# Kernel tuning notes

Hardware: AMD Instinct MI355X
Metric: run time of the kernel (lower is better)

The kernel has to match this reference:

```python
import jax, jax.numpy as jnp
import numpy as np

B, N, K = 2, 10000, 20
C_EDGE = [(4, 64), (64, 64), (64, 128), (128, 128)]  # (Cin, Cout) per edge conv
C_CAT = 64 + 64 + 128 + 128  # 384
C5 = 512
C_FEAT = [128, 128, 256]
NUM_CLASSES = 20


def _neighbor_idx(n, k):
    # idx[i] = torch.roll(arange(n), shifts=i)[:k]  ->  idx[i, j] = (j - i) mod n
    return (jnp.arange(k)[None, :] - jnp.arange(n)[:, None]) % n  # (N, K)


def _edge_conv(x, w, s, t, idx):
    # x: (B, C, N); w: (Co, 2C); s, t: (Co,) folded eval-mode BN scale/shift
    xn = x[:, :, idx]                                  # neighbor gather (B, C, N, K)
    ctr = jnp.broadcast_to(x[:, :, :, None], xn.shape)  # center repeat (B, C, N, K)
    e = jnp.concatenate([ctr - xn, ctr], axis=1)        # edge feature (B, 2C, N, K)
    y = jnp.einsum('oc,bcnk->bonk', w, e)               # 1x1 conv
    y = y * s[None, :, None, None] + t[None, :, None, None]
    y = jnp.where(y > 0, y, 0.2 * y)                    # LeakyReLU(0.2)
    return jnp.max(y, axis=-1)                          # max over K -> (B, Co, N)


def _conv1d_bn(x, w, s, t):
    # x: (B, C, N); 1x1 conv1d + folded BN
    return jnp.einsum('oc,bcn->bon', w, x) * s[None, :, None] + t[None, :, None]


def setup_inputs() -> dict:
    key = jax.random.key(0)
    ks = iter(jax.random.split(key, 64))
    d = {
        'coords': jax.random.normal(next(ks), (B, N, 3), jnp.float32),
        'feats': jax.random.normal(next(ks), (B, N, 4), jnp.float32),
    }
    def conv_bn(cin, cout):
        w = jax.random.normal(next(ks), (cout, cin), jnp.float32) / np.sqrt(cin).astype(np.float32)
        s = 0.75 + 0.5 * jax.random.uniform(next(ks), (cout,), jnp.float32)
        t = 0.1 * jax.random.normal(next(ks), (cout,), jnp.float32)
        return w, s, t
    for i, (ci, co) in enumerate(C_EDGE, 1):
        d[f'ew{i}'], d[f'es{i}'], d[f'et{i}'] = conv_bn(2 * ci, co)
    d['w5'], d['s5'], d['t5'] = conv_bn(C_CAT, C5)
    for i, cf in enumerate(C_FEAT, 1):
        d[f'fw{i}'], d[f'fs{i}'], d[f'ft{i}'] = conv_bn(C5, cf)
    d['sem_w'] = jax.random.normal(next(ks), (NUM_CLASSES, C_FEAT[-1]), jnp.float32) / np.sqrt(C_FEAT[-1]).astype(np.float32)
    d['sem_b'] = jnp.zeros((NUM_CLASSES,), jnp.float32)
    return d


def reference(coords, feats,
              ew1, es1, et1, ew2, es2, et2, ew3, es3, et3, ew4, es4, et4,
              w5, s5, t5,
              fw1, fs1, ft1, fw2, fs2, ft2, fw3, fs3, ft3,
              sem_w, sem_b):
    # x = cat(coords, intensity) -> (B, 4, N)
    x = jnp.concatenate([coords, feats[:, :, 3:4]], axis=-1).transpose(0, 2, 1)
    idx = _neighbor_idx(N, K)
    x1 = _edge_conv(x, ew1, es1, et1, idx)
    x2 = _edge_conv(x1, ew2, es2, et2, idx)
    x3 = _edge_conv(x2, ew3, es3, et3, idx)
    x4 = _edge_conv(x3, ew4, es4, et4, idx)
    xc = jnp.concatenate([x1, x2, x3, x4], axis=1)       # (B, 384, N)
    y = _conv1d_bn(xc, w5, s5, t5)
    y = jnp.where(y > 0, y, 0.2 * y)                      # conv5 activation
    f1 = _conv1d_bn(y, fw1, fs1, ft1).transpose(0, 2, 1)  # (B, N, 128)
    f2 = _conv1d_bn(y, fw2, fs2, ft2).transpose(0, 2, 1)  # (B, N, 128)
    f3 = _conv1d_bn(y, fw3, fs3, ft3).transpose(0, 2, 1)  # (B, N, 256)
    sem_logits = f3 @ sem_w.T + sem_b                     # (B, N, 20)
    masks = jnp.zeros((B, N), dtype=bool)                 # no padding: N == num_points
    return (f1, f2, f3, coords, masks, sem_logits)
```

## Files before the change

kernel.cpp:

```cpp
#include <hip/hip_runtime.h>

#define N_PTS 10000
#define NBATCH 2
#define COLS (N_PTS * NBATCH)
#define COLSP 20096

typedef __attribute__((ext_vector_type(8))) short bf16x8;
typedef __attribute__((ext_vector_type(4))) float f32x4;

static __device__ __forceinline__ float leaky(float v) { return v > 0.f ? v : 0.2f * v; }

static __device__ __forceinline__ unsigned short f2b(float x) {
  unsigned int u = __float_as_uint(x);
  unsigned int r = (u + 0x7fffu + ((u >> 16) & 1u)) >> 16;
  return (unsigned short)r;
}
static __device__ __forceinline__ float b2f(unsigned short h) {
  return __uint_as_float((unsigned int)h << 16);
}

static __device__ __forceinline__ void prep_one(const float* __restrict__ ew,
                                                float* __restrict__ WS, int O, int C, int i) {
  int o = i / C, c = i - o * C;
  float wa = ew[(size_t)o * 2 * C + c];
  float wb = ew[(size_t)o * 2 * C + C + c];
  WS[(size_t)o * C + c] = wa + wb;
  WS[(size_t)(O + o) * C + c] = wa;
}

__global__ void prep_all(const float* __restrict__ coords, const float* __restrict__ feats,
                         float* __restrict__ X0, const float* __restrict__ ew1,
                         float* __restrict__ WS1, const float* __restrict__ ew2,
                         float* __restrict__ WS2, const float* __restrict__ ew3,
                         float* __restrict__ WS3, const float* __restrict__ ew4,
                         float* __restrict__ WS4) {
  int i = blockIdx.x * 256 + threadIdx.x;
  if (i < COLS) {
    const float* cp = coords + (size_t)i * 3;
    X0[0 * COLS + i] = cp[0];
    X0[1 * COLS + i] = cp[1];
    X0[2 * COLS + i] = cp[2];
    X0[3 * COLS + i] = feats[(size_t)i * 4 + 3];
    return;
  }
  i -= COLS;
  if (i < 256) { prep_one(ew1, WS1, 64, 4, i); return; }
  i -= 256;
  if (i < 4096) { prep_one(ew2, WS2, 64, 64, i); return; }
  i -= 4096;
  if (i < 8192) { prep_one(ew3, WS3, 128, 64, i); return; }
  i -= 8192;
  if (i < 16384) { prep_one(ew4, WS4, 128, 128, i); return; }
}

template <int K, int MODE>
__global__ __launch_bounds__(256) void gemm_kernel(
    const float* __restrict__ W, const float* __restrict__ X, float* __restrict__ Out,
    const float* __restrict__ s, const float* __restrict__ t, int Cf) {
  __shared__ float Ws[32][68];
  __shared__ float Xs[32][132];
  const int tid = threadIdx.x;
  const int col0 = blockIdx.x * 128;
  const int row0 = blockIdx.y * 64;
  const int tn = tid & 31, tm = tid >> 5;
  float acc[8][4];
#pragma unroll
  for (int i = 0; i < 8; i++)
#pragma unroll
    for (int j = 0; j < 4; j++) acc[i][j] = 0.f;

  const bool colok = (col0 + tn * 4) < COLS;

  for (int k0 = 0; k0 < K; k0 += 32) {
    {
      int m = tid >> 2;
      int kq = (tid & 3) * 8;
      if ((K & 31) == 0) {
        const float* wp = W + (size_t)(row0 + m) * K + k0 + kq;
        float4 w0 = *(const float4*)wp;
        float4 w1 = *(const float4*)(wp + 4);
        Ws[kq + 0][m] = w0.x; Ws[kq + 1][m] = w0.y; Ws[kq + 2][m] = w0.z; Ws[kq + 3][m] = w0.w;
        Ws[kq + 4][m] = w1.x; Ws[kq + 5][m] = w1.y; Ws[kq + 6][m] = w1.z; Ws[kq + 7][m] = w1.w;
      } else {
#pragma unroll
        for (int j = 0; j < 8; j++) {
          int k = kq + j;
          Ws[k][m] = (k0 + k < K) ? W[(size_t)(row0 + m) * K + k0 + k] : 0.f;
        }
      }
    }
#pragma unroll
    for (int p = 0; p < 4; p++) {
      int idx = tid + p * 256;
      int k = idx >> 5;
      int n4 = (idx & 31) << 2;
      int col = col0 + n4;
      float4 v = make_float4(0.f, 0.f, 0.f, 0.f);
      if (k0 + k < K && col < COLS) v = *(const float4*)(X + (size_t)(k0 + k) * COLS + col);
      *(float4*)&Xs[k][n4] = v;
    }
    __syncthreads();
#pragma unroll
    for (int k = 0; k < 32; k++) {
      float a[8], b[4];
      *(float4*)&a[0] = *(const float4*)&Ws[k][tm * 8];
      *(float4*)&a[4] = *(const float4*)&Ws[k][tm * 8 + 4];
      *(float4*)&b[0] = *(const float4*)&Xs[k][tn * 4];
#pragma unroll
      for (int i = 0; i < 8; i++)
#pragma unroll
        for (int j = 0; j < 4; j++) acc[i][j] = fmaf(a[i], b[j], acc[i][j]);
    }
    __syncthreads();
  }

  if (colok) {
#pragma unroll
    for (int i = 0; i < 8; i++) {
      int row = row0 + tm * 8 + i;
      float4 v = make_float4(acc[i][0], acc[i][1], acc[i][2], acc[i][3]);
      *(float4*)(Out + (size_t)row * COLS + col0 + tn * 4) = v;
    }
  }
}

__global__ __launch_bounds__(256) void edge_finish(const float* __restrict__ AB, int O,
                                                   const float* __restrict__ s,
                                                   const float* __restrict__ t,
                                                   float* __restrict__ Xout) {
  __shared__ float sh[1024 + 20];
  int o = blockIdx.y;
  int b = blockIdx.z;
  int n0 = blockIdx.x * 1024;
  int nb = min(1024, N_PTS - n0);
  const float* Bt = AB + (size_t)(O + o) * COLS + (size_t)b * N_PTS;
  int base = N_PTS - n0 - nb + 1;
  int L = nb + 19;
  for (int i = threadIdx.x; i < L; i += 256) {
    int p = base + i;
    if (p >= N_PTS) p -= N_PTS;
    sh[i] = Bt[p];
  }
  __syncthreads();
  const float* Arow = AB + (size_t)o * COLS + (size_t)b * N_PTS;
  float ss = s[o], tt = t[o];
  for (int d = threadIdx.x; d < nb; d += 256) {
    int w = nb - 1 - d;
    float mn = sh[w];
#pragma unroll
    for (int k = 1; k < 20; k++) mn = fminf(mn, sh[w + k]);
    float v = (Arow[n0 + d] - mn) * ss + tt;
    Xout[(size_t)o * COLS + (size_t)b * N_PTS + n0 + d] = leaky(v);
  }
}

__global__ void sem_prep(const float* __restrict__ sem_w, const float* __restrict__ sem_b,
                         const float* __restrict__ fw3, const float* __restrict__ fs3,
                         const float* __restrict__ ft3, float* __restrict__ SWp,
                         float* __restrict__ biasp) {
  int i = blockIdx.x * blockDim.x + threadIdx.x;
  if (i < 20 * 512) {
    int cls = i / 512, k = i - cls * 512;
    float acc = 0.f;
    for (int c = 0; c < 256; c++) acc += sem_w[cls * 256 + c] * fs3[c] * fw3[(size_t)c * 512 + k];
    SWp[i] = acc;
  }
  if (i < 20) {
    float acc = sem_b[i];
    for (int c = 0; c < 256; c++) acc += sem_w[i * 256 + c] * ft3[c];
    biasp[i] = acc;
  }
}

__global__ void split_w5(const float* __restrict__ w5, unsigned short* __restrict__ Wc) {
  int i = blockIdx.x * 256 + threadIdx.x;
  if (i >= 512 * 384) return;
  int m = i / 384, k = i - m * 384;
  float w = w5[i];
  unsigned short hi = f2b(w);
  unsigned short lo = f2b(w - b2f(hi));
  unsigned short* row = Wc + (size_t)m * 1152;
  row[k] = hi;
  row[384 + k] = hi;
  row[768 + k] = lo;
}

__global__ void split_wf(const float* __restrict__ fw1, const float* __restrict__ fw2,
                         const float* __restrict__ fw3, const float* __restrict__ SWp,
                         const float* __restrict__ fs1, const float* __restrict__ ft1,
                         const float* __restrict__ fs2, const float* __restrict__ ft2,
                         const float* __restrict__ fs3, const float* __restrict__ ft3,
                         const float* __restrict__ Bp, unsigned short* __restrict__ Wc,
                         float* __restrict__ sF, float* __restrict__ tF) {
  int i = blockIdx.x * 256 + threadIdx.x;
  if (i >= 640 * 512) return;
  int m = i >> 9, k = i & 511;
  float w = 0.f, sv = 0.f, tv = 0.f;
  if (m < 128) {
    w = fw1[(size_t)m * 512 + k]; sv = fs1[m]; tv = ft1[m];
  } else if (m < 256) {
    w = fw2[(size_t)(m - 128) * 512 + k]; sv = fs2[m - 128]; tv = ft2[m - 128];
  } else if (m < 512) {
    w = fw3[(size_t)(m - 256) * 512 + k]; sv = fs3[m - 256]; tv = ft3[m - 256];
  } else if (m < 532) {
    w = SWp[(size_t)(m - 512) * 512 + k]; sv = 1.f; tv = Bp[m - 512];
  }
  unsigned short hi = f2b(w);
  unsigned short lo = f2b(w - b2f(hi));
  unsigned short* row = Wc + (size_t)m * 1536;
  row[k] = hi;
  row[512 + k] = hi;
  row[1024 + k] = lo;
  if (k == 0) { sF[m] = sv; tF[m] = tv; }
}

__global__ __launch_bounds__(256) void xpose_split(const float* __restrict__ XC,
                                                   unsigned short* __restrict__ XCt) {
  __shared__ float tile[32][65];
  int n0 = blockIdx.x * 64;
  int c0 = blockIdx.y * 32;
#pragma unroll
  for (int i = 0; i < 8; i++) {
    int e = threadIdx.x + i * 256;
    int c = e >> 6, n = e & 63;
    float v = 0.f;
    if (n0 + n < COLS) v = XC[(size_t)(c0 + c) * COLS + n0 + n];
    tile[c][n] = v;
  }
  __syncthreads();
#pragma unroll
  for (int i = 0; i < 2; i++) {
    int e = threadIdx.x + i * 256;
    int n = e >> 3, cq = (e & 7) * 4;
    if (n0 + n >= COLS) continue;
    unsigned short h[4], l[4];
#pragma unroll
    for (int j = 0; j < 4; j++) {
      float v = tile[cq + j][n];
      h[j] = f2b(v);
      l[j] = f2b(v - b2f(h[j]));
    }
    unsigned short* op = XCt + (size_t)(n0 + n) * 768 + c0 + cq;
    *(ushort4*)op = make_ushort4(h[0], h[1], h[2], h[3]);
    *(ushort4*)(op + 384) = make_ushort4(l[0], l[1], l[2], l[3]);
  }
}

template <int KP, int KX, int XSTR, int MODE>
__global__ __launch_bounds__(256) void mgemm(
    const unsigned short* __restrict__ Wc, const unsigned short* __restrict__ Xt,
    float* __restrict__ O0, float* __restrict__ O1, float* __restrict__ O2,
    float* __restrict__ O3, unsigned short* __restrict__ Yt, const float* __restrict__ s,
    const float* __restrict__ t) {
  __shared__ unsigned short Al[128 * 32];
  __shared__ unsigned short Bl[128 * 32];
  const int tid = threadIdx.x;
  const int wid = tid >> 6, lane = tid & 63;
  const int col0 = blockIdx.x * 128;
  const int row0 = blockIdx.y * 128;
  const int wm = wid >> 1, wn = wid & 1;
  f32x4 acc[4][4];
  f32x4 z = {0.f, 0.f, 0.f, 0.f};
#pragma unroll
  for (int i = 0; i < 4; i++)
#pragma unroll
    for (int j = 0; j < 4; j++) acc[i][j] = z;

  for (int k0 = 0; k0 < KP; k0 += 32) {
    int xoff = (k0 < 2 * KX) ? k0 : k0 - 2 * KX;
#pragma unroll
    for (int p = 0; p < 2; p++) {
      int idx = tid + p * 256;
      int r = idx >> 2, jj = idx & 3;
      int js = jj ^ ((r >> 1) & 3);
      __builtin_amdgcn_global_load_lds(
          (const __attribute__((address_space(1))) unsigned int*)(Wc + (size_t)(row0 + r) * KP +
                                                                  k0 + js * 8),
          (__attribute__((address_space(3))) unsigned int*)(Al + idx * 8), 16, 0, 0);
      __builtin_amdgcn_global_load_lds(
          (const __attribute__((address_space(1))) unsigned int*)(Xt + (size_t)(col0 + r) * XSTR +
                                                                  xoff + js * 8),
          (__attribute__((address_space(3))) unsigned int*)(Bl + idx * 8), 16, 0, 0);
    }
    __syncthreads();
    bf16x8 a[4], b[4];
#pragma unroll
    for (int f = 0; f < 4; f++) {
      int m = wm * 64 + f * 16 + (lane & 15);
      int ja = (lane >> 4) ^ ((m >> 1) & 3);
      a[f] = *(const bf16x8*)(Al + m * 32 + ja * 8);
      int n = wn * 64 + f * 16 + (lane & 15);
      int jb = (lane >> 4) ^ ((n >> 1) & 3);
      b[f] = *(const bf16x8*)(Bl + n * 32 + jb * 8);
    }
#pragma unroll
    for (int i = 0; i < 4; i++)
#pragma unroll
      for (int j = 0; j < 4; j++)
        acc[i][j] = __builtin_amdgcn_mfma_f32_16x16x32_bf16(a[i], b[j], acc[i][j], 0, 0, 0);
    __syncthreads();
  }

#pragma unroll
  for (int j = 0; j < 4; j++) {
    int n = col0 + wn * 64 + j * 16 + (lane & 15);
    if (n >= COLS) continue;
#pragma unroll
    for (int i = 0; i < 4; i++) {
      int mb = row0 + wm * 64 + i * 16 + 4 * (lane >> 4);
      if (MODE == 0) {
        unsigned short h[4], l[4];
#pragma unroll
        for (int r = 0; r < 4; r++) {
          float v = acc[i][j][r] * s[mb + r] + t[mb + r];
          v = leaky(v);
          h[r] = f2b(v);
          l[r] = f2b(v - b2f(h[r]));
        }
        unsigned short* yp = Yt + (size_t)n * 1024 + mb;
        *(ushort4*)yp = make_ushort4(h[0], h[1], h[2], h[3]);
        *(ushort4*)(yp + 512) = make_ushort4(l[0], l[1], l[2], l[3]);
      } else {
        float4 v;
        v.x = acc[i][j][0] * s[mb + 0] + t[mb + 0];
        v.y = acc[i][j][1] * s[mb + 1] + t[mb + 1];
        v.z = acc[i][j][2] * s[mb + 2] + t[mb + 2];
        v.w = acc[i][j][3] * s[mb + 3] + t[mb + 3];
        float* p;
        if (mb < 128)
          p = O0 + (size_t)n * 128 + mb;
        else if (mb < 256)
          p = O1 + (size_t)n * 128 + (mb - 128);
        else if (mb < 512)
          p = O2 + (size_t)n * 256 + (mb - 256);
        else if (mb < 532)
          p = O3 + (size_t)n * 20 + (mb - 512);
        else
          continue;
        *(float4*)p = v;
      }
    }
  }
}

__global__ void misc_kernel(const float* __restrict__ coords, float* __restrict__ out_coords,
                            float* __restrict__ out_masks) {
  int i = blockIdx.x * blockDim.x + threadIdx.x;
  if (i < NBATCH * N_PTS * 3) out_coords[i] = coords[i];
  if (i < NBATCH * N_PTS) out_masks[i] = 0.f;
}

extern "C" void kernel_launch(void* const* d_in, const int* in_sizes, int n_in, void* d_out,
                              int out_size, void* d_ws, size_t ws_size, hipStream_t stream) {
  const float* coords = (const float*)d_in[0];
  const float* feats = (const float*)d_in[1];
  const float* ew1 = (const float*)d_in[2];
  const float* es1 = (const float*)d_in[3];
  const float* et1 = (const float*)d_in[4];
  const float* ew2 = (const float*)d_in[5];
  const float* es2 = (const float*)d_in[6];
  const float* et2 = (const float*)d_in[7];
  const float* ew3 = (const float*)d_in[8];
  const float* es3 = (const float*)d_in[9];
  const float* et3 = (const float*)d_in[10];
  const float* ew4 = (const float*)d_in[11];
  const float* es4 = (const float*)d_in[12];
  const float* et4 = (const float*)d_in[13];
  const float* w5 = (const float*)d_in[14];
  const float* s5 = (const float*)d_in[15];
  const float* t5 = (const float*)d_in[16];
  const float* fw1 = (const float*)d_in[17];
  const float* fs1 = (const float*)d_in[18];
  const float* ft1 = (const float*)d_in[19];
  const float* fw2 = (const float*)d_in[20];
  const float* fs2 = (const float*)d_in[21];
  const float* ft2 = (const float*)d_in[22];
  const float* fw3 = (const float*)d_in[23];
  const float* fs3 = (const float*)d_in[24];
  const float* ft3 = (const float*)d_in[25];
  const float* sem_w = (const float*)d_in[26];
  const float* sem_b = (const float*)d_in[27];
  float* out = (float*)d_out;
  float* ws = (float*)d_ws;

  float* X0 = ws;
  float* WS1 = ws + 80000;
  float* WS2 = ws + 80512;
  float* WS3 = ws + 88704;
  float* WS4 = ws + 105088;
  float* sF = ws + 137856;
  float* tF = ws + 138496;
  float* SWp = ws + 139136;
  float* Bp = ws + 149376;
  unsigned short* Wc5 = (unsigned short*)(ws + 149440);
  unsigned short* WcF = (unsigned short*)(ws + 444352);
  unsigned short* XCt = (unsigned short*)(ws + 935872);
  float* AB = ws + 8652736;
  float* XC = ws + 13772736;
  unsigned short* Y5t = (unsigned short*)(ws + 8652736);

  float* out_f1 = out;
  float* out_f2 = out + 2560000;
  float* out_f3 = out + 5120000;
  float* out_coords = out + 10240000;
  float* out_masks = out + 10300000;
  float* out_sem = out + 10320000;

  dim3 blk(256);
  const int GX = (COLS + 127) / 128;

  prep_all<<<dim3(192), blk, 0, stream>>>(coords, feats, X0, ew1, WS1, ew2, WS2, ew3, WS3, ew4,
                                          WS4);

  gemm_kernel<4, 0><<<dim3(GX, 2), blk, 0, stream>>>(WS1, X0, AB, nullptr, nullptr, 0);
  edge_finish<<<dim3(10, 64, 2), blk, 0, stream>>>(AB, 64, es1, et1, XC);
  gemm_kernel<64, 0><<<dim3(GX, 2), blk, 0, stream>>>(WS2, XC, AB, nullptr, nullptr, 0);
  edge_finish<<<dim3(10, 64, 2), blk, 0, stream>>>(AB, 64, es2, et2, XC + (size_t)64 * COLS);
  gemm_kernel<64, 0><<<dim3(GX, 4), blk, 0, stream>>>(WS3, XC + (size_t)64 * COLS, AB, nullptr,
                                                      nullptr, 0);
  edge_finish<<<dim3(10, 128, 2), blk, 0, stream>>>(AB, 128, es3, et3, XC + (size_t)128 * COLS);
  gemm_kernel<128, 0><<<dim3(GX, 4), blk, 0, stream>>>(WS4, XC + (size_t)128 * COLS, AB, nullptr,
                                                       nullptr, 0);
  edge_finish<<<dim3(10, 128, 2), blk, 0, stream>>>(AB, 128, es4, et4, XC + (size_t)256 * COLS);

  split_w5<<<dim3(768), blk, 0, stream>>>(w5, Wc5);
  sem_prep<<<dim3(40), blk, 0, stream>>>(sem_w, sem_b, fw3, fs3, ft3, SWp, Bp);
  split_wf<<<dim3(1280), blk, 0, stream>>>(fw1, fw2, fw3, SWp, fs1, ft1, fs2, ft2, fs3, ft3, Bp,
                                           WcF, sF, tF);

  xpose_split<<<dim3(313, 12), blk, 0, stream>>>(XC, XCt);

  mgemm<1152, 384, 768, 0><<<dim3(GX, 4), blk, 0, stream>>>(Wc5, XCt, nullptr, nullptr, nullptr,
                                                            nullptr, Y5t, s5, t5);

  mgemm<1536, 512, 1024, 1><<<dim3(GX, 5), blk, 0, stream>>>(WcF, Y5t, out_f1, out_f2, out_f3,
                                                             out_sem, nullptr, sF, tF);

  misc_kernel<<<dim3(236), blk, 0, stream>>>(coords, out_coords, out_masks);
}
```

Before: 397.4 us.

## Triple-buffer LDS tiles in mgemm with asynchronous prefetch two stages ahead

The mgemm main loop now keeps three LDS buffers per operand and issues the global_load_lds copies for tile k+2 while computing tile k. A manual s_waitcnt vmcnt plus a single barrier per iteration replaces the two __syncthreads per tile. The goal is to hide global-memory latency behind the MFMA work and cut barrier count. In exchange, LDS use per block triples, which can lower occupancy. Correctness depends on the exact count of outstanding loads per stage.

```diff
diff --git a/kernel.cpp b/kernel.cpp
--- a/kernel.cpp
+++ b/kernel.cpp
@@ -3,7 +3,6 @@
 #define N_PTS 10000
 #define NBATCH 2
 #define COLS (N_PTS * NBATCH)
-#define COLSP 20096
 
 typedef __attribute__((ext_vector_type(8))) short bf16x8;
 typedef __attribute__((ext_vector_type(4))) float f32x4;
@@ -252,8 +251,8 @@
     float* __restrict__ O0, float* __restrict__ O1, float* __restrict__ O2,
     float* __restrict__ O3, unsigned short* __restrict__ Yt, const float* __restrict__ s,
     const float* __restrict__ t) {
-  __shared__ unsigned short Al[128 * 32];
-  __shared__ unsigned short Bl[128 * 32];
+  __shared__ unsigned short Al[3][128 * 32];
+  __shared__ unsigned short Bl[3][128 * 32];
   const int tid = threadIdx.x;
   const int wid = tid >> 6, lane = tid & 63;
   const int col0 = blockIdx.x * 128;
@@ -266,8 +265,11 @@
 #pragma unroll
     for (int j = 0; j < 4; j++) acc[i][j] = z;
 
-  for (int k0 = 0; k0 < KP; k0 += 32) {
-    int xoff = (k0 < 2 * KX) ? k0 : k0 - 2 * KX;
+  constexpr int NT = KP / 32;
+
+  auto stage = [&](int buf, int kst) {
+    int k0s = kst * 32;
+    int xoffs = (k0s < 2 * KX) ? k0s : k0s - 2 * KX;
 #pragma unroll
     for (int p = 0; p < 2; p++) {
       int idx = tid + p * 256;
@@ -275,31 +277,45 @@
       int js = jj ^ ((r >> 1) & 3);
       __builtin_amdgcn_global_load_lds(
           (const __attribute__((address_space(1))) unsigned int*)(Wc + (size_t)(row0 + r) * KP +
-                                                                  k0 + js * 8),
-          (__attribute__((address_space(3))) unsigned int*)(Al + idx * 8), 16, 0, 0);
+                                                                  k0s + js * 8),
+          (__attribute__((address_space(3))) unsigned int*)(&Al[buf][idx * 8]), 16, 0, 0);
       __builtin_amdgcn_global_load_lds(
           (const __attribute__((address_space(1))) unsigned int*)(Xt + (size_t)(col0 + r) * XSTR +
-                                                                  xoff + js * 8),
-          (__attribute__((address_space(3))) unsigned int*)(Bl + idx * 8), 16, 0, 0);
-    }
-    __syncthreads();
+                                                                  xoffs + js * 8),
+          (__attribute__((address_space(3))) unsigned int*)(&Bl[buf][idx * 8]), 16, 0, 0);
+    }
+  };
+
+  auto compute = [&](int buf) {
     bf16x8 a[4], b[4];
 #pragma unroll
     for (int f = 0; f < 4; f++) {
       int m = wm * 64 + f * 16 + (lane & 15);
       int ja = (lane >> 4) ^ ((m >> 1) & 3);
-      a[f] = *(const bf16x8*)(Al + m * 32 + ja * 8);
+      a[f] = *(const bf16x8*)(&Al[buf][m * 32 + ja * 8]);
       int n = wn * 64 + f * 16 + (lane & 15);
       int jb = (lane >> 4) ^ ((n >> 1) & 3);
-      b[f] = *(const bf16x8*)(Bl + n * 32 + jb * 8);
+      b[f] = *(const bf16x8*)(&Bl[buf][n * 32 + jb * 8]);
     }
 #pragma unroll
     for (int i = 0; i < 4; i++)
 #pragma unroll
       for (int j = 0; j < 4; j++)
         acc[i][j] = __builtin_amdgcn_mfma_f32_16x16x32_bf16(a[i], b[j], acc[i][j], 0, 0, 0);
-    __syncthreads();
-  }
+  };
+
+  stage(0, 0);
+  stage(1, 1);
+#pragma unroll 1
+  for (int tt = 0; tt < NT - 1; ++tt) {
+    asm volatile("s_waitcnt vmcnt(4)" ::: "memory");
+    __builtin_amdgcn_s_barrier();
+    if (tt + 2 < NT) stage((tt + 2) % 3, tt + 2);
+    compute(tt % 3);
+  }
+  asm volatile("s_waitcnt vmcnt(0)" ::: "memory");
+  __builtin_amdgcn_s_barrier();
+  compute((NT - 1) % 3);
 
 #pragma unroll
   for (int j = 0; j < 4; j++) {
```

New measurement: 387.5 us. -2.5%, faster.
